# Kernel optimization log

Hardware: AMD Instinct MI355X
Metric: run time of the kernel (lower is better)

## Reference

```python
import jax, jax.numpy as jnp
import numpy as np


def setup_inputs() -> dict:
    key = jax.random.key(0)
    k1, k2, k3 = jax.random.split(key, 3)
    B, F, H, W = 16, 16, 256, 256
    inp = jax.random.normal(k1, (B, F, H, W), dtype=jnp.float32)
    target = jax.random.normal(k2, (B, F, H, W), dtype=jnp.float32)
    masks = jax.random.randint(k3, (B, F, H, W), 0, 2).astype(jnp.bool_)
    hull = jnp.zeros((1,), dtype=jnp.int32)  # unused by the module's forward
    return {"input": inp, "target": target, "masks": masks, "hull": hull}


def _masked_mean_per_feature(diff, w):
    # diff: [B,F,H,W]; w: float mask broadcastable to diff. Returns [F] masked means
    # with 0.0 where the mask is empty (matching the torch `if len(diff) > 0` guard).
    s = jnp.sum(diff * w, axis=(0, 2, 3))                               # [F]
    c = jnp.sum(jnp.broadcast_to(w, diff.shape), axis=(0, 2, 3))        # [F]
    return jnp.where(c > 0, s / jnp.maximum(c, 1.0), 0.0)


def reference(input, target, masks, hull):
    diff = jnp.abs(input - target)                                      # [B,F,H,W]
    m = masks.astype(diff.dtype)                                        # feature masks
    m_not = 1.0 - m                                                     # background
    m_all = jnp.any(masks, axis=1, keepdims=True).astype(diff.dtype)    # [B,1,H,W]

    loss_features = jnp.mean(_masked_mean_per_feature(diff, m))
    loss_background = jnp.mean(_masked_mean_per_feature(diff, m_not))
    loss_all_features = jnp.mean(_masked_mean_per_feature(diff, m_all))

    return (loss_features + loss_all_features + loss_background) / 3.0
```

## Files before the change

### kernel.cpp

```cpp
#include <hip/hip_runtime.h>

constexpr int B = 16, F = 16, H = 256, W = 256;
constexpr int HW = H * W;
constexpr int SPATIAL = B * HW;
constexpr int PLANE4 = HW / 4;
constexpr int BSTRIDE4 = F * PLANE4;

constexpr int NBLK = 2048;
constexpr int NTHREADS = 256;
constexpr int NWAVES = NTHREADS / 64;
constexpr int G = 2;
constexpr int TOT4 = B * PLANE4;
static_assert(NBLK * G * 64 == TOT4, "coverage must be exact");

constexpr int NVALS = 50;

__global__ __launch_bounds__(NTHREADS) void heatloss_main(
        const float4* __restrict__ inp, const float4* __restrict__ tgt,
        const unsigned int* __restrict__ msk, float* __restrict__ partials) {
    const int tid  = threadIdx.x;
    const int wave = tid >> 6;
    const int lane = tid & 63;
    const int foff = (wave * 4) * PLANE4;

    float s[4]  = {0.f, 0.f, 0.f, 0.f};
    float c[4]  = {0.f, 0.f, 0.f, 0.f};
    float dt[4] = {0.f, 0.f, 0.f, 0.f};
    float sall = 0.f, call = 0.f;

    __shared__ unsigned int anybuf[2][NWAVES][64];

    #pragma unroll
    for (int it = 0; it < G; ++it) {
        const int slot = blockIdx.x * G + it;
        const int gidx = slot * 64 + lane;
        const int b    = gidx >> 14;
        const int hw4  = gidx & (PLANE4 - 1);
        const int base = b * BSTRIDE4 + foff + hw4;

        unsigned int m[4];
        float4 av[4], tv[4];
        #pragma unroll
        for (int j = 0; j < 4; j++) m[j] = msk[base + j * PLANE4];
        #pragma unroll
        for (int j = 0; j < 4; j++) av[j] = inp[base + j * PLANE4];
        #pragma unroll
        for (int j = 0; j < 4; j++) tv[j] = tgt[base + j * PLANE4];

        const unsigned int anyw = m[0] | m[1] | m[2] | m[3];
        anybuf[it & 1][wave][lane] = anyw;
        __syncthreads();
        const unsigned int any = anybuf[it & 1][0][lane] | anybuf[it & 1][1][lane]
                               | anybuf[it & 1][2][lane] | anybuf[it & 1][3][lane];

        const float af0 = (any & 0x000000FFu) ? 1.f : 0.f;
        const float af1 = (any & 0x0000FF00u) ? 1.f : 0.f;
        const float af2 = (any & 0x00FF0000u) ? 1.f : 0.f;
        const float af3 = (any & 0xFF000000u) ? 1.f : 0.f;
        if (wave == 0) call += (af0 + af1) + (af2 + af3);

        #pragma unroll
        for (int j = 0; j < 4; j++) {
            const float4 a = av[j];
            const float4 t = tv[j];
            const float d0 = fabsf(a.x - t.x);
            const float d1 = fabsf(a.y - t.y);
            const float d2 = fabsf(a.z - t.z);
            const float d3 = fabsf(a.w - t.w);
            const unsigned int mm = m[j];
            const float m0 = (float)( mm        & 0xFFu);
            const float m1 = (float)((mm >> 8)  & 0xFFu);
            const float m2 = (float)((mm >> 16) & 0xFFu);
            const float m3 = (float)( mm >> 24);
            dt[j] += (d0 + d1) + (d2 + d3);
            s[j]  += m0 * d0 + m1 * d1 + m2 * d2 + m3 * d3;
            c[j]  += (m0 + m1) + (m2 + m3);
            sall  += af0 * d0 + af1 * d1 + af2 * d2 + af3 * d3;
        }
    }

    __shared__ float red[NWAVES][14];
    #pragma unroll
    for (int j = 0; j < 4; j++) {
        float xs = s[j], xc = c[j], xd = dt[j];
        #pragma unroll
        for (int o = 32; o > 0; o >>= 1) {
            xs += __shfl_down(xs, o, 64);
            xc += __shfl_down(xc, o, 64);
            xd += __shfl_down(xd, o, 64);
        }
        if (lane == 0) {
            red[wave][0 + j] = xs;
            red[wave][4 + j] = xc;
            red[wave][8 + j] = xd;
        }
    }
    float xa = sall, xcl = call;
    #pragma unroll
    for (int o = 32; o > 0; o >>= 1) {
        xa  += __shfl_down(xa,  o, 64);
        xcl += __shfl_down(xcl, o, 64);
    }
    if (lane == 0) { red[wave][12] = xa; red[wave][13] = xcl; }
    __syncthreads();

    if (tid < NVALS) {
        float t;
        if (tid < 16) {
            t = red[tid >> 2][0 + (tid & 3)];
        } else if (tid < 32) {
            const int f = tid - 16;
            t = red[f >> 2][4 + (f & 3)];
        } else if (tid < 48) {
            const int f = tid - 32;
            t = red[f >> 2][8 + (f & 3)];
        } else if (tid == 48) {
            t = (red[0][12] + red[1][12]) + (red[2][12] + red[3][12]);
        } else {
            t = (red[0][13] + red[1][13]) + (red[2][13] + red[3][13]);
        }
        partials[tid * NBLK + blockIdx.x] = t;
    }
}

__global__ __launch_bounds__(NTHREADS) void heatloss_final(
        const float* __restrict__ partials, float* __restrict__ out) {
    const int tid  = threadIdx.x;
    const int wave = tid >> 6;
    const int lane = tid & 63;
    __shared__ float vals[NVALS];
    for (int v = wave; v < NVALS; v += NWAVES) {
        const float* p = partials + v * NBLK;
        float x = 0.f;
        #pragma unroll
        for (int k = 0; k < NBLK / 64; k++) x += p[lane + k * 64];
        #pragma unroll
        for (int o = 32; o > 0; o >>= 1) x += __shfl_down(x, o, 64);
        if (lane == 0) vals[v] = x;
    }
    __syncthreads();
    if (tid == 0) {
        const float Nf = (float)SPATIAL;
        float lf = 0.f, lbg = 0.f;
        #pragma unroll
        for (int f = 0; f < F; f++) {
            const float sf = vals[f], cf = vals[16 + f], dtf = vals[32 + f];
            lf += (cf > 0.f) ? sf / cf : 0.f;
            const float sbg = dtf - sf, cbg = Nf - cf;
            lbg += (cbg > 0.f) ? sbg / cbg : 0.f;
        }
        const float sa = vals[48], cl = vals[49];
        const float lall = (cl > 0.f) ? sa / cl : 0.f;
        out[0] = (lf / 16.f + lbg / 16.f + lall / 16.f) / 3.f;
    }
}

extern "C" void kernel_launch(void* const* d_in, const int* in_sizes, int n_in,
                              void* d_out, int out_size, void* d_ws, size_t ws_size,
                              hipStream_t stream) {
    const float4*       inp = (const float4*)d_in[0];
    const float4*       tgt = (const float4*)d_in[1];
    const unsigned int* msk = (const unsigned int*)d_in[2];
    float* out      = (float*)d_out;
    float* partials = (float*)d_ws;

    heatloss_main<<<NBLK, NTHREADS, 0, stream>>>(inp, tgt, msk, partials);
    heatloss_final<<<1, NTHREADS, 0, stream>>>(partials, out);
}
```

Measured before the change: 192.1 us.

## Stream loads through LDS with async global_load_lds double buffering

Replaces the direct register loads with asynchronous global-to-LDS loads (global_load_lds) into a per-wave double buffer, and overlaps the fetch of the next tile with compute on the current one using explicit vmcnt waits and barriers. Halves the block count and doubles the tiles per block, so each block runs a longer pipeline. The any-mask is read straight from the shared mask buffers, which removes the separate anybuf exchange. This adds about 72KB of LDS per block, which limits occupancy, and it depends on the hand-written vmcnt counts being correct.

```diff
diff --git a/kernel.cpp b/kernel.cpp
--- a/kernel.cpp
+++ b/kernel.cpp
@@ -6,52 +6,69 @@
 constexpr int PLANE4 = HW / 4;
 constexpr int BSTRIDE4 = F * PLANE4;
 
-constexpr int NBLK = 2048;
+constexpr int NBLK = 1024;
 constexpr int NTHREADS = 256;
 constexpr int NWAVES = NTHREADS / 64;
-constexpr int G = 2;
-constexpr int TOT4 = B * PLANE4;
-static_assert(NBLK * G * 64 == TOT4, "coverage must be exact");
+constexpr int G = 4;
+static_assert(NBLK * G * 64 == B * PLANE4, "coverage must be exact");
 
 constexpr int NVALS = 50;
+constexpr int WBUF = 9216;
+
+
+__device__ __forceinline__ void g2l16(const float4* g, void* l) {
+    __builtin_amdgcn_global_load_lds((__attribute__((address_space(1))) void*)g,
+                                     (__attribute__((address_space(3))) void*)l,
+                                     16, 0, 0);
+}
+__device__ __forceinline__ void g2l4(const unsigned int* g, void* l) {
+    __builtin_amdgcn_global_load_lds((__attribute__((address_space(1))) void*)g,
+                                     (__attribute__((address_space(3))) void*)l,
+                                     4, 0, 0);
+}
 
 __global__ __launch_bounds__(NTHREADS) void heatloss_main(
         const float4* __restrict__ inp, const float4* __restrict__ tgt,
         const unsigned int* __restrict__ msk, float* __restrict__ partials) {
+    __shared__ __align__(16) unsigned char lds[NWAVES][2][WBUF];
+    __shared__ float red[NWAVES][14];
+
     const int tid  = threadIdx.x;
     const int wave = tid >> 6;
     const int lane = tid & 63;
     const int foff = (wave * 4) * PLANE4;
 
+    const int run0 = blockIdx.x * (G * 64);
+    const int b    = run0 >> 14;
+    const int hw40 = run0 & (PLANE4 - 1);
+    const int gbase = b * BSTRIDE4 + foff + hw40 + lane;
+    const float4*       ga = inp + gbase;
+    const float4*       gt = tgt + gbase;
+    const unsigned int* gm = msk + gbase;
+
     float s[4]  = {0.f, 0.f, 0.f, 0.f};
     float c[4]  = {0.f, 0.f, 0.f, 0.f};
     float dt[4] = {0.f, 0.f, 0.f, 0.f};
     float sall = 0.f, call = 0.f;
 
-    __shared__ unsigned int anybuf[2][NWAVES][64];
-
-    #pragma unroll
-    for (int it = 0; it < G; ++it) {
-        const int slot = blockIdx.x * G + it;
-        const int gidx = slot * 64 + lane;
-        const int b    = gidx >> 14;
-        const int hw4  = gidx & (PLANE4 - 1);
-        const int base = b * BSTRIDE4 + foff + hw4;
-
-        unsigned int m[4];
-        float4 av[4], tv[4];
-        #pragma unroll
-        for (int j = 0; j < 4; j++) m[j] = msk[base + j * PLANE4];
-        #pragma unroll
-        for (int j = 0; j < 4; j++) av[j] = inp[base + j * PLANE4];
-        #pragma unroll
-        for (int j = 0; j < 4; j++) tv[j] = tgt[base + j * PLANE4];
-
-        const unsigned int anyw = m[0] | m[1] | m[2] | m[3];
-        anybuf[it & 1][wave][lane] = anyw;
-        __syncthreads();
-        const unsigned int any = anybuf[it & 1][0][lane] | anybuf[it & 1][1][lane]
-                               | anybuf[it & 1][2][lane] | anybuf[it & 1][3][lane];
+    auto stage = [&](int t, int buf) {
+        unsigned char* dst = &lds[wave][buf][0];
+        const int off = t * 64;
+        #pragma unroll
+        for (int j = 0; j < 4; j++) g2l16(ga + off + j * PLANE4, dst + j * 1024);
+        #pragma unroll
+        for (int j = 0; j < 4; j++) g2l16(gt + off + j * PLANE4, dst + 4096 + j * 1024);
+        #pragma unroll
+        for (int j = 0; j < 4; j++) g2l4 (gm + off + j * PLANE4, dst + 8192 + j * 256);
+    };
+
+    auto consume = [&](int buf) {
+        unsigned int any = 0u;
+        #pragma unroll
+        for (int w2 = 0; w2 < 4; w2++)
+            #pragma unroll
+            for (int j = 0; j < 4; j++)
+                any |= *(const unsigned int*)&lds[w2][buf][8192 + j * 256 + lane * 4];
 
         const float af0 = (any & 0x000000FFu) ? 1.f : 0.f;
         const float af1 = (any & 0x0000FF00u) ? 1.f : 0.f;
@@ -61,13 +78,14 @@
 
         #pragma unroll
         for (int j = 0; j < 4; j++) {
-            const float4 a = av[j];
-            const float4 t = tv[j];
-            const float d0 = fabsf(a.x - t.x);
-            const float d1 = fabsf(a.y - t.y);
-            const float d2 = fabsf(a.z - t.z);
-            const float d3 = fabsf(a.w - t.w);
-            const unsigned int mm = m[j];
+            const float4 a  = *(const float4*)&lds[wave][buf][j * 1024 + lane * 16];
+            const float4 t4 = *(const float4*)&lds[wave][buf][4096 + j * 1024 + lane * 16];
+            const unsigned int mm =
+                *(const unsigned int*)&lds[wave][buf][8192 + j * 256 + lane * 4];
+            const float d0 = fabsf(a.x - t4.x);
+            const float d1 = fabsf(a.y - t4.y);
+            const float d2 = fabsf(a.z - t4.z);
+            const float d3 = fabsf(a.w - t4.w);
             const float m0 = (float)( mm        & 0xFFu);
             const float m1 = (float)((mm >> 8)  & 0xFFu);
             const float m2 = (float)((mm >> 16) & 0xFFu);
@@ -77,9 +95,25 @@
             c[j]  += (m0 + m1) + (m2 + m3);
             sall  += af0 * d0 + af1 * d1 + af2 * d2 + af3 * d3;
         }
-    }
-
-    __shared__ float red[NWAVES][14];
+    };
+
+    stage(0, 0);
+    #pragma unroll
+    for (int t = 0; t < G; ++t) {
+        if (t + 1 < G) {
+            stage(t + 1, (t + 1) & 1);
+            asm volatile("s_waitcnt vmcnt(12)" ::: "memory");
+        } else {
+            asm volatile("s_waitcnt vmcnt(0)" ::: "memory");
+        }
+        __builtin_amdgcn_s_barrier();
+        consume(t & 1);
+        if (t + 1 < G) {
+            asm volatile("" ::: "memory");
+            __builtin_amdgcn_s_barrier();
+        }
+    }
+
     #pragma unroll
     for (int j = 0; j < 4; j++) {
         float xs = s[j], xc = c[j], xd = dt[j];
```

New measurement: 199.1 us. 1.04x slower.
